# Performance work log

Hardware: AMD Instinct MI355X
Metric: run time of the kernel (lower is better)

Reference implementation:

```python
import jax, jax.numpy as jnp
import numpy as np

BN_EPS = 1e-5


def setup_inputs() -> dict:
    key = jax.random.key(0)
    ks = jax.random.split(key, 10)
    N, E, D = 100000, 1600000, 64
    node_feats = jax.random.normal(ks[0], (N, D), dtype=jnp.float32)
    edge_feats = jax.random.randint(ks[1], (E, 3), 0, 2, dtype=jnp.int64)
    edge_index = jax.random.randint(ks[2], (2, E), 0, N, dtype=jnp.int64)
    return {
        "node_feats": node_feats,
        "edge_feats": edge_feats,
        "edge_index": edge_index,
        "num_nodes": N,
        "num_edges": E,
        "eps": jnp.zeros((1,), jnp.float32),
        "bond_emb0": jax.random.normal(ks[3], (5, D), dtype=jnp.float32) * 0.05,
        "bond_emb1": jax.random.normal(ks[4], (6, D), dtype=jnp.float32) * 0.05,
        "bond_emb2": jax.random.normal(ks[5], (2, D), dtype=jnp.float32) * 0.05,
        "W1": jax.random.normal(ks[6], (2 * D, D), dtype=jnp.float32) * (1.0 / np.sqrt(D)),
        "b1": jnp.zeros((2 * D,), jnp.float32),
        "gamma": jnp.ones((2 * D,), jnp.float32),
        "beta": jnp.zeros((2 * D,), jnp.float32),
        "W2": jax.random.normal(ks[7], (D, 2 * D), dtype=jnp.float32) * (1.0 / np.sqrt(2 * D)),
        "b2": jnp.zeros((D,), jnp.float32),
    }


def reference(node_feats, edge_feats, edge_index, num_nodes, num_edges,
              eps, bond_emb0, bond_emb1, bond_emb2,
              W1, b1, gamma, beta, W2, b2):
    # BondEncoder: sum of categorical embeddings over 3 bond features -> [E, D]
    edge_emb = (bond_emb0[edge_feats[:, 0]]
                + bond_emb1[edge_feats[:, 1]]
                + bond_emb2[edge_feats[:, 2]])
    # gather source-node feats (edge_index[1]), combine, relu -> [E, D]
    message = jax.nn.relu(node_feats[edge_index[1]] + edge_emb)
    # scatter_add into target nodes (edge_index[0]) -> [N, D]
    message_reduce = jax.ops.segment_sum(message, edge_index[0], num_segments=num_nodes)
    h = (1.0 + eps) * node_feats + message_reduce  # eps shape [1] broadcasts
    # MLP: Linear -> BatchNorm1d (training-mode batch stats) -> ReLU -> Linear
    h1 = h @ W1.T + b1  # [N, 2D]
    mean = jnp.mean(h1, axis=0)
    var = jnp.mean(jnp.square(h1 - mean), axis=0)  # biased variance (torch BN)
    h1 = gamma * (h1 - mean) * jax.lax.rsqrt(var + BN_EPS) + beta
    h1 = jax.nn.relu(h1)
    return h1 @ W2.T + b2  # [N, D]
```

## Files before the change

kernel.cpp:

```cpp
#include <hip/hip_runtime.h>
#include <stdint.h>

#define D    64
#define D2   128
#define R    98
#define NBK  1024
#define CAP  2176

__global__ void k_embsum(
    const float* __restrict__ be0, const float* __restrict__ be1,
    const float* __restrict__ be2, float* __restrict__ embsum,
    int* __restrict__ bcursor, float* __restrict__ Mbar)
{
    int c = blockIdx.x;
    int t = threadIdx.x;
    if (c < 60) {
        int f0 = c / 12;
        int r  = c % 12;
        int f1 = r / 2;
        int f2 = r % 2;
        embsum[c * D + t] = be0[f0 * D + t] + be1[f1 * D + t] + be2[f2 * D + t];
    } else if (c < 76) {
        int i = (c - 60) * 64 + t;
        if (i < NBK) bcursor[i * 16] = i * CAP;
    } else {
        int i = (c - 76) * 64 + t;
        Mbar[i] = 0.0f;
    }
}

__global__ __launch_bounds__(512) void k_part(
    const int* __restrict__ ei, const int* __restrict__ ef,
    int* __restrict__ bcursor, int* __restrict__ payload, int E)
{
    __shared__ int scnt[NBK];
    __shared__ int sstart[NBK];
    __shared__ int sgbase[NBK];
    __shared__ int sdat[4096];
    __shared__ unsigned short sbkt[4096];
    __shared__ int sred2[512];

    int t = threadIdx.x;
    for (int i = t; i < NBK; i += 512) scnt[i] = 0;
    __syncthreads();

    int base2 = blockIdx.x * 2048;

    int b0[4], p0[4], r0[4];
    int b1[4], p1[4], r1[4];

    #pragma unroll
    for (int k = 0; k < 4; k++) {
        int i2 = base2 + k * 512 + t;
        int e0 = i2 * 2;
        if (e0 < E) {
            int2 d  = ((const int2*)ei)[i2];
            int2 s  = ((const int2*)(ei + E))[i2];
            int2 q0 = ((const int2*)ef)[3 * i2 + 0];
            int2 q1 = ((const int2*)ef)[3 * i2 + 1];
            int2 q2 = ((const int2*)ef)[3 * i2 + 2];
            {
                int bb = d.x / R; if (bb > NBK - 1) bb = NBK - 1;
                int ld = d.x - bb * R;
                int code = q0.x * 12 + q0.y * 2 + q1.x;
                b0[k] = bb;
                p0[k] = s.x | (code << 17) | (ld << 23);
                r0[k] = atomicAdd(&scnt[bb], 1);
            }
            if (e0 + 1 < E) {
                int bb = d.y / R; if (bb > NBK - 1) bb = NBK - 1;
                int ld = d.y - bb * R;
                int code = q1.y * 12 + q2.x * 2 + q2.y;
                b1[k] = bb;
                p1[k] = s.y | (code << 17) | (ld << 23);
                r1[k] = atomicAdd(&scnt[bb], 1);
            }
        }
    }
    __syncthreads();

    int c0 = scnt[t * 2], c1 = scnt[t * 2 + 1];
    sred2[t] = c0 + c1;
    __syncthreads();
    int sv = sred2[t];
    for (int off = 1; off < 512; off <<= 1) {
        int x = (t >= off) ? sred2[t - off] : 0;
        __syncthreads();
        sred2[t] += x;
        __syncthreads();
    }
    int excl = sred2[t] - sv;
    sstart[t * 2]     = excl;
    sstart[t * 2 + 1] = excl + c0;
    __syncthreads();

    for (int i = t; i < NBK; i += 512) {
        int c = scnt[i];
        if (c) sgbase[i] = atomicAdd(&bcursor[i * 16], c);
    }
    __syncthreads();

    #pragma unroll
    for (int k = 0; k < 4; k++) {
        int i2 = base2 + k * 512 + t;
        int e0 = i2 * 2;
        if (e0 < E) {
            int slot = sstart[b0[k]] + r0[k];
            sdat[slot] = p0[k]; sbkt[slot] = (unsigned short)b0[k];
            if (e0 + 1 < E) {
                slot = sstart[b1[k]] + r1[k];
                sdat[slot] = p1[k]; sbkt[slot] = (unsigned short)b1[k];
            }
        }
    }
    __syncthreads();

    int tc = E - base2 * 2; if (tc > 4096) tc = 4096;
    #pragma unroll
    for (int k = 0; k < 8; k++) {
        int i = k * 512 + t;
        if (i < tc) {
            int bb = sbkt[i];
            int pos = sgbase[bb] + (i - sstart[bb]);
            if (pos < (bb + 1) * CAP) payload[pos] = sdat[i];
        }
    }
}

__global__ __launch_bounds__(512, 8) void k_sortred(
    const float* __restrict__ nf,
    const int* __restrict__ bcursor,
    int* __restrict__ payload,
    const float* __restrict__ embsum,
    const float* __restrict__ epsp,
    float* __restrict__ h, int N)
{
    __shared__ float sE[60 * D];
    __shared__ int   sq[CAP];
    __shared__ int   scn[R + 1];
    __shared__ int   scur[R];
    __shared__ int   sscan[128];

    int tid = threadIdx.x;
    int b = blockIdx.x;
    int n0 = b * R;

    for (int i = tid; i < 60 * D; i += 512) sE[i] = embsum[i];
    if (tid <= R) scn[tid] = 0;
    __syncthreads();

    int js = b * CAP;
    int cnt = bcursor[b * 16] - js;
    if (cnt > CAP) cnt = CAP;
    if (cnt < 0) cnt = 0;

    for (int i = tid; i < cnt; i += 512)
        atomicAdd(&scn[((unsigned)payload[js + i] >> 23) + 1], 1);
    __syncthreads();

    if (tid < 128) sscan[tid] = (tid <= R) ? scn[tid] : 0;
    __syncthreads();
    for (int off = 1; off < 128; off <<= 1) {
        int x = 0;
        if (tid < 128 && tid >= off) x = sscan[tid - off];
        __syncthreads();
        if (tid < 128) sscan[tid] += x;
        __syncthreads();
    }
    if (tid <= R) {
        scn[tid] = sscan[tid];
        if (tid < R) scur[tid] = sscan[tid];
    }
    __syncthreads();

    for (int i = tid; i < cnt; i += 512) {
        int u = payload[js + i];
        int pos = atomicAdd(&scur[(unsigned)u >> 23], 1);
        sq[pos] = u;
    }
    __syncthreads();

    int w = tid >> 6, l = tid & 63;
    float epsv = 1.0f + epsp[0];
    for (int r = w; r < R; r += 8) {
        int n = n0 + r;
        if (n >= N) break;
        int st = scn[r], en = scn[r + 1];
        float acc = 0.0f;
        for (int jb = st; jb < en; jb += 64) {
            int u = (jb + l < en) ? sq[jb + l] : 0;
            int m = en - jb; if (m > 64) m = 64;
            int t = 0;
            for (; t + 8 <= m; t += 8) {
                int a0 = __shfl(u, t + 0);
                int a1 = __shfl(u, t + 1);
                int a2 = __shfl(u, t + 2);
                int a3 = __shfl(u, t + 3);
                int a4 = __shfl(u, t + 4);
                int a5 = __shfl(u, t + 5);
                int a6 = __shfl(u, t + 6);
                int a7 = __shfl(u, t + 7);
                float x0 = nf[(size_t)(a0 & 0x1FFFF) * D + l];
                float x1 = nf[(size_t)(a1 & 0x1FFFF) * D + l];
                float x2 = nf[(size_t)(a2 & 0x1FFFF) * D + l];
                float x3 = nf[(size_t)(a3 & 0x1FFFF) * D + l];
                float x4 = nf[(size_t)(a4 & 0x1FFFF) * D + l];
                float x5 = nf[(size_t)(a5 & 0x1FFFF) * D + l];
                float x6 = nf[(size_t)(a6 & 0x1FFFF) * D + l];
                float x7 = nf[(size_t)(a7 & 0x1FFFF) * D + l];
                float e0 = sE[((a0 >> 17) & 63) * D + l];
                float e1 = sE[((a1 >> 17) & 63) * D + l];
                float e2 = sE[((a2 >> 17) & 63) * D + l];
                float e3 = sE[((a3 >> 17) & 63) * D + l];
                float e4 = sE[((a4 >> 17) & 63) * D + l];
                float e5 = sE[((a5 >> 17) & 63) * D + l];
                float e6 = sE[((a6 >> 17) & 63) * D + l];
                float e7 = sE[((a7 >> 17) & 63) * D + l];
                acc += fmaxf(x0 + e0, 0.0f) + fmaxf(x1 + e1, 0.0f)
                     + fmaxf(x2 + e2, 0.0f) + fmaxf(x3 + e3, 0.0f)
                     + fmaxf(x4 + e4, 0.0f) + fmaxf(x5 + e5, 0.0f)
                     + fmaxf(x6 + e6, 0.0f) + fmaxf(x7 + e7, 0.0f);
            }
            for (; t + 4 <= m; t += 4) {
                int a0 = __shfl(u, t + 0);
                int a1 = __shfl(u, t + 1);
                int a2 = __shfl(u, t + 2);
                int a3 = __shfl(u, t + 3);
                float x0 = nf[(size_t)(a0 & 0x1FFFF) * D + l];
                float x1 = nf[(size_t)(a1 & 0x1FFFF) * D + l];
                float x2 = nf[(size_t)(a2 & 0x1FFFF) * D + l];
                float x3 = nf[(size_t)(a3 & 0x1FFFF) * D + l];
                float e0 = sE[((a0 >> 17) & 63) * D + l];
                float e1 = sE[((a1 >> 17) & 63) * D + l];
                float e2 = sE[((a2 >> 17) & 63) * D + l];
                float e3 = sE[((a3 >> 17) & 63) * D + l];
                acc += fmaxf(x0 + e0, 0.0f) + fmaxf(x1 + e1, 0.0f)
                     + fmaxf(x2 + e2, 0.0f) + fmaxf(x3 + e3, 0.0f);
            }
            for (; t < m; t++) {
                int a = __shfl(u, t);
                acc += fmaxf(nf[(size_t)(a & 0x1FFFF) * D + l]
                             + sE[((a >> 17) & 63) * D + l], 0.0f);
            }
        }
        h[(size_t)n * D + l] = fmaf(epsv, nf[(size_t)n * D + l], acc);
    }
    __syncthreads();

    float* P = (float*)(payload + (size_t)b * CAP);
    const float4* h4 = (const float4*)h;
    if (tid < 256) {
        int iB = tid >> 4, jB = tid & 15;
        float M[4][4];
        #pragma unroll
        for (int a = 0; a < 4; a++)
            #pragma unroll
            for (int c = 0; c < 4; c++) M[a][c] = 0.0f;
        #pragma unroll 2
        for (int n2 = 0; n2 < R; n2++) {
            int n = n0 + n2;
            if (n >= N) break;
            float4 a = h4[(size_t)n * 16 + iB];
            float4 c = h4[(size_t)n * 16 + jB];
            M[0][0] = fmaf(a.x, c.x, M[0][0]);
            M[0][1] = fmaf(a.x, c.y, M[0][1]);
            M[0][2] = fmaf(a.x, c.z, M[0][2]);
            M[0][3] = fmaf(a.x, c.w, M[0][3]);
            M[1][0] = fmaf(a.y, c.x, M[1][0]);
            M[1][1] = fmaf(a.y, c.y, M[1][1]);
            M[1][2] = fmaf(a.y, c.z, M[1][2]);
            M[1][3] = fmaf(a.y, c.w, M[1][3]);
            M[2][0] = fmaf(a.z, c.x, M[2][0]);
            M[2][1] = fmaf(a.z, c.y, M[2][1]);
            M[2][2] = fmaf(a.z, c.z, M[2][2]);
            M[2][3] = fmaf(a.z, c.w, M[2][3]);
            M[3][0] = fmaf(a.w, c.x, M[3][0]);
            M[3][1] = fmaf(a.w, c.y, M[3][1]);
            M[3][2] = fmaf(a.w, c.z, M[3][2]);
            M[3][3] = fmaf(a.w, c.w, M[3][3]);
        }
        #pragma unroll
        for (int a = 0; a < 4; a++)
            #pragma unroll
            for (int c = 0; c < 4; c++) {
                int gi = iB * 4 + a, gj = jB * 4 + c;
                if (gi <= gj)
                    P[gi * 64 + gj - ((gi * (gi + 1)) >> 1)] = M[a][c];
            }
    } else if (tid < 320) {
        int lc = tid - 256;
        float s = 0.0f;
        for (int n2 = 0; n2 < R; n2++) {
            int n = n0 + n2;
            if (n >= N) break;
            s += h[(size_t)n * D + lc];
        }
        P[2080 + lc] = s;
    }
}

__global__ __launch_bounds__(512) void k_redM(
    const float* __restrict__ pM,
    float* __restrict__ Mbar, float invN)
{
    __shared__ float sred[512];
    int tid = threadIdx.x;
    int eq = tid & 63, bq = tid >> 6;
    int ec = blockIdx.x >> 2;
    int qg = blockIdx.x & 3;
    int e  = ec * 64 + eq;

    int src;
    if (e < 4096) {
        int i = e >> 6, j = e & 63;
        int a = i < j ? i : j;
        int b2 = i < j ? j : i;
        src = a * 64 + b2 - ((a * (a + 1)) >> 1);
    } else {
        src = 2080 + (e - 4096);
    }

    int bbase = qg * 256;
    float s0 = 0.0f, s1 = 0.0f, s2 = 0.0f, s3 = 0.0f;
    for (int b = bq; b < 256; b += 32) {
        s0 += pM[(size_t)(bbase + b +  0) * CAP + src];
        s1 += pM[(size_t)(bbase + b +  8) * CAP + src];
        s2 += pM[(size_t)(bbase + b + 16) * CAP + src];
        s3 += pM[(size_t)(bbase + b + 24) * CAP + src];
    }
    sred[tid] = (s0 + s1) + (s2 + s3);
    __syncthreads();
    if (tid < 64) {
        float s = 0.0f;
        #pragma unroll
        for (int q = 0; q < 8; q++) s += sred[q * 64 + tid];
        atomicAdd(&Mbar[e], s * invN);
    }
}

__global__ __launch_bounds__(64) void k_bn(
    const float* __restrict__ Mbar,
    const float* __restrict__ W1,
    const float* __restrict__ b1,
    const float* __restrict__ gamma, const float* __restrict__ beta,
    float* __restrict__ ss)
{
    int c = blockIdx.x;
    int k = threadIdx.x;

    float wk = W1[c * D + k];
    float dk = wk * Mbar[4096 + k];

    float tk = 0.0f;
    #pragma unroll 8
    for (int j = 0; j < 64; j++)
        tk = fmaf(Mbar[k * 64 + j], W1[c * D + j], tk);
    float qk = wk * tk;

    #pragma unroll
    for (int off = 32; off > 0; off >>= 1) {
        dk += __shfl_xor(dk, off);
        qk += __shfl_xor(qk, off);
    }

    if (k == 0) {
        float var  = fmaxf(qk - dk * dk, 0.0f);
        float mean = dk + b1[c];
        float sc   = gamma[c] * rsqrtf(var + 1e-5f);
        ss[c]       = sc;
        ss[128 + c] = beta[c] - mean * sc;
    }
}

#define ABS 132
__global__ __launch_bounds__(512) void k_gemm2(
    const float* __restrict__ h,
    const float* __restrict__ W1,
    const float* __restrict__ b1,
    const float* __restrict__ ss,
    const float* __restrict__ W2,
    const float* __restrict__ b2v,
    float* __restrict__ out,
    int N, int tiles)
{
    __shared__ float AB[128 * ABS];
    __shared__ float W1t[64 * 128];
    __shared__ float W2t[128 * 64];

    int tid = threadIdx.x;

    {
        int c  = tid >> 2;
        int k0 = (tid & 3) * 16;
        const float4* wr = (const float4*)(W1 + c * D + k0);
        #pragma unroll
        for (int q = 0; q < 4; q++) {
            float4 u = wr[q];
            int k = k0 + q * 4;
            W1t[(k + 0) * 128 + c] = u.x;
            W1t[(k + 1) * 128 + c] = u.y;
            W1t[(k + 2) * 128 + c] = u.z;
            W1t[(k + 3) * 128 + c] = u.w;
        }
    }
    {
        int j  = tid >> 3;
        int k0 = (tid & 7) * 16;
        const float4* wr = (const float4*)(W2 + j * D2 + k0);
        #pragma unroll
        for (int q = 0; q < 4; q++) {
            float4 u = wr[q];
            int k = k0 + q * 4;
            W2t[(k + 0) * 64 + j] = u.x;
            W2t[(k + 1) * 64 + j] = u.y;
            W2t[(k + 2) * 64 + j] = u.z;
            W2t[(k + 3) * 64 + j] = u.w;
        }
    }

    int rg = tid >> 5, cg = tid & 31;
    float bb0 = b1[cg * 4 + 0];
    float bb1 = b1[cg * 4 + 1];
    float bb2 = b1[cg * 4 + 2];
    float bb3 = b1[cg * 4 + 3];
    float4 scv = *(const float4*)&ss[cg * 4];
    float4 shv = *(const float4*)&ss[128 + cg * 4];

    int r2 = tid >> 4, c2 = tid & 15;
    float4 obv = *(const float4*)&b2v[c2 * 4];

    int sr = tid >> 2;
    int sc16 = (tid & 3) * 16;

    float4 pf[4];
    #pragma unroll
    for (int q = 0; q < 4; q++) pf[q] = make_float4(0.f, 0.f, 0.f, 0.f);
    {
        int gr = blockIdx.x * 128 + sr;
        if (gr < N) {
            const float4* hrow = (const float4*)(h + (size_t)gr * D + sc16);
            #pragma unroll
            for (int q = 0; q < 4; q++) pf[q] = hrow[q];
        }
    }

    for (int t = blockIdx.x; t < tiles; t += gridDim.x) {
        int row0 = t * 128;
        __syncthreads();
        {
            float* dstp = &AB[sr * ABS + sc16];
            #pragma unroll
            for (int q = 0; q < 4; q++) ((float4*)dstp)[q] = pf[q];
        }
        __syncthreads();

        float acc[8][4];
        #pragma unroll
        for (int i = 0; i < 8; i++)
            #pragma unroll
            for (int j = 0; j < 4; j++) acc[i][j] = 0.0f;

        #pragma unroll 2
        for (int k4 = 0; k4 < 16; k4++) {
            float4 w0 = *(const float4*)&W1t[(k4 * 4 + 0) * 128 + cg * 4];
            float4 w1 = *(const float4*)&W1t[(k4 * 4 + 1) * 128 + cg * 4];
            float4 w2 = *(const float4*)&W1t[(k4 * 4 + 2) * 128 + cg * 4];
            float4 w3 = *(const float4*)&W1t[(k4 * 4 + 3) * 128 + cg * 4];
            #pragma unroll
            for (int i = 0; i < 8; i++) {
                float4 a = *(const float4*)&AB[(rg * 8 + i) * ABS + k4 * 4];
                acc[i][0] = fmaf(a.x, w0.x, acc[i][0]);
                acc[i][1] = fmaf(a.x, w0.y, acc[i][1]);
                acc[i][2] = fmaf(a.x, w0.z, acc[i][2]);
                acc[i][3] = fmaf(a.x, w0.w, acc[i][3]);
                acc[i][0] = fmaf(a.y, w1.x, acc[i][0]);
                acc[i][1] = fmaf(a.y, w1.y, acc[i][1]);
                acc[i][2] = fmaf(a.y, w1.z, acc[i][2]);
                acc[i][3] = fmaf(a.y, w1.w, acc[i][3]);
                acc[i][0] = fmaf(a.z, w2.x, acc[i][0]);
                acc[i][1] = fmaf(a.z, w2.y, acc[i][1]);
                acc[i][2] = fmaf(a.z, w2.z, acc[i][2]);
                acc[i][3] = fmaf(a.z, w2.w, acc[i][3]);
                acc[i][0] = fmaf(a.w, w3.x, acc[i][0]);
                acc[i][1] = fmaf(a.w, w3.y, acc[i][1]);
                acc[i][2] = fmaf(a.w, w3.z, acc[i][2]);
                acc[i][3] = fmaf(a.w, w3.w, acc[i][3]);
            }
        }
        __syncthreads();

        int tn = t + gridDim.x;
        #pragma unroll
        for (int q = 0; q < 4; q++) pf[q] = make_float4(0.f, 0.f, 0.f, 0.f);
        if (tn < tiles) {
            int gr = tn * 128 + sr;
            if (gr < N) {
                const float4* hrow = (const float4*)(h + (size_t)gr * D + sc16);
                #pragma unroll
                for (int q = 0; q < 4; q++) pf[q] = hrow[q];
            }
        }

        #pragma unroll
        for (int i = 0; i < 8; i++) {
            float g0 = fmaxf(fmaf(acc[i][0] + bb0, scv.x, shv.x), 0.0f);
            float g1 = fmaxf(fmaf(acc[i][1] + bb1, scv.y, shv.y), 0.0f);
            float g2 = fmaxf(fmaf(acc[i][2] + bb2, scv.z, shv.z), 0.0f);
            float g3 = fmaxf(fmaf(acc[i][3] + bb3, scv.w, shv.w), 0.0f);
            *(float4*)&AB[(rg * 8 + i) * ABS + cg * 4] = make_float4(g0, g1, g2, g3);
        }
        __syncthreads();

        float acc2[4][4];
        #pragma unroll
        for (int i = 0; i < 4; i++)
            #pragma unroll
            for (int j = 0; j < 4; j++) acc2[i][j] = 0.0f;

        #pragma unroll 2
        for (int k4 = 0; k4 < 32; k4++) {
            float4 u0 = *(const float4*)&W2t[(k4 * 4 + 0) * 64 + c2 * 4];
            float4 u1 = *(const float4*)&W2t[(k4 * 4 + 1) * 64 + c2 * 4];
            float4 u2 = *(const float4*)&W2t[(k4 * 4 + 2) * 64 + c2 * 4];
            float4 u3 = *(const float4*)&W2t[(k4 * 4 + 3) * 64 + c2 * 4];
            #pragma unroll
            for (int i = 0; i < 4; i++) {
                float4 g = *(const float4*)&AB[(r2 * 4 + i) * ABS + k4 * 4];
                acc2[i][0] = fmaf(g.x, u0.x, acc2[i][0]);
                acc2[i][1] = fmaf(g.x, u0.y, acc2[i][1]);
                acc2[i][2] = fmaf(g.x, u0.z, acc2[i][2]);
                acc2[i][3] = fmaf(g.x, u0.w, acc2[i][3]);
                acc2[i][0] = fmaf(g.y, u1.x, acc2[i][0]);
                acc2[i][1] = fmaf(g.y, u1.y, acc2[i][1]);
                acc2[i][2] = fmaf(g.y, u1.z, acc2[i][2]);
                acc2[i][3] = fmaf(g.y, u1.w, acc2[i][3]);
                acc2[i][0] = fmaf(g.z, u2.x, acc2[i][0]);
                acc2[i][1] = fmaf(g.z, u2.y, acc2[i][1]);
                acc2[i][2] = fmaf(g.z, u2.z, acc2[i][2]);
                acc2[i][3] = fmaf(g.z, u2.w, acc2[i][3]);
                acc2[i][0] = fmaf(g.w, u3.x, acc2[i][0]);
                acc2[i][1] = fmaf(g.w, u3.y, acc2[i][1]);
                acc2[i][2] = fmaf(g.w, u3.z, acc2[i][2]);
                acc2[i][3] = fmaf(g.w, u3.w, acc2[i][3]);
            }
        }

        #pragma unroll
        for (int i = 0; i < 4; i++) {
            int gr = row0 + r2 * 4 + i;
            if (gr < N) {
                float4 pk = make_float4(acc2[i][0] + obv.x, acc2[i][1] + obv.y,
                                        acc2[i][2] + obv.z, acc2[i][3] + obv.w);
                *(float4*)&out[(size_t)gr * D + c2 * 4] = pk;
            }
        }
    }
}

extern "C" void kernel_launch(void* const* d_in, const int* in_sizes, int n_in,
                              void* d_out, int out_size, void* d_ws, size_t ws_size,
                              hipStream_t stream)
{
    const float* nf    = (const float*)d_in[0];
    const int*   ef    = (const int*)d_in[1];
    const int*   ei    = (const int*)d_in[2];
    const float* epsp  = (const float*)d_in[5];
    const float* be0   = (const float*)d_in[6];
    const float* be1   = (const float*)d_in[7];
    const float* be2   = (const float*)d_in[8];
    const float* W1    = (const float*)d_in[9];
    const float* b1    = (const float*)d_in[10];
    const float* gamma = (const float*)d_in[11];
    const float* beta  = (const float*)d_in[12];
    const float* W2    = (const float*)d_in[13];
    const float* b2v   = (const float*)d_in[14];
    float*       out   = (float*)d_out;

    int N = in_sizes[0] / D;
    int E = in_sizes[1] / 3;

    int tiles2 = (N + 127) / 128;

    float* h       = (float*)d_ws;
    float* Mbar    = h + (size_t)N * D;
    float* ss      = Mbar + 4224;
    float* embsum  = ss + 256;
    int*   bcursor = (int*)(embsum + 60 * D);
    int*   payload = bcursor + NBK * 16;
    float* pM      = (float*)payload;

    k_embsum<<<142, 64, 0, stream>>>(be0, be1, be2, embsum, bcursor, Mbar);

    int E2 = (E + 1) / 2;
    int gP = (E2 + 2047) / 2048;
    k_part<<<gP, 512, 0, stream>>>(ei, ef, bcursor, payload, E);

    k_sortred<<<NBK, 512, 0, stream>>>(nf, bcursor, payload, embsum, epsp, h, N);

    k_redM<<<260, 512, 0, stream>>>(pM, Mbar, 1.0f / (float)N);
    k_bn<<<128, 64, 0, stream>>>(Mbar, W1, b1, gamma, beta, ss);

    k_gemm2<<<256, 512, 0, stream>>>(h, W1, b1, ss, W2, b2v, out, N, tiles2);
}
```

Before: 306.5 us.

## Pre-transpose MLP weights globally, restructure GEMM tiling to wave-uniform weight loads

The W1/W2 transposes move into the setup kernel, which writes them to global workspace, so the fused MLP kernel no longer stages weights in LDS. Each wave now owns a fixed column slice and reads its weights as wave-uniform global loads that hit cache. Each thread handles two rows, and the grid doubles because LDS use per block drops. The edge partition kernel also switches to 8 contiguous edges per thread with int4 vector loads. The risk is higher per-thread register pressure and extra global traffic for the weight reads.

```diff
diff --git a/kernel.cpp b/kernel.cpp
--- a/kernel.cpp
+++ b/kernel.cpp
@@ -10,7 +10,9 @@
 __global__ void k_embsum(
     const float* __restrict__ be0, const float* __restrict__ be1,
     const float* __restrict__ be2, float* __restrict__ embsum,
-    int* __restrict__ bcursor, float* __restrict__ Mbar)
+    int* __restrict__ bcursor, float* __restrict__ Mbar,
+    const float* __restrict__ W1, const float* __restrict__ W2,
+    float* __restrict__ W1tg, float* __restrict__ W2tg)
 {
     int c = blockIdx.x;
     int t = threadIdx.x;
@@ -23,9 +25,16 @@
     } else if (c < 76) {
         int i = (c - 60) * 64 + t;
         if (i < NBK) bcursor[i * 16] = i * CAP;
-    } else {
+    } else if (c < 142) {
         int i = (c - 76) * 64 + t;
         Mbar[i] = 0.0f;
+    } else if (c < 270) {
+        int ch = c - 142;
+        W1tg[t * 128 + ch] = W1[ch * D + t];
+    } else {
+        int j = c - 270;
+        W2tg[t * 64 + j]        = W2[j * D2 + t];
+        W2tg[(t + 64) * 64 + j] = W2[j * D2 + t + 64];
     }
 }
 
@@ -44,37 +53,52 @@
     for (int i = t; i < NBK; i += 512) scnt[i] = 0;
     __syncthreads();
 
-    int base2 = blockIdx.x * 2048;
-
-    int b0[4], p0[4], r0[4];
-    int b1[4], p1[4], r1[4];
+    int e0 = blockIdx.x * 4096 + t * 8;
+    int dd[8], sv[8], fa[8], fb[8], fc[8];
+    int bk[8], pk[8], rk[8];
+
+    if (e0 + 8 <= E) {
+        int4 dA = *(const int4*)(ei + e0);
+        int4 dB = *(const int4*)(ei + e0 + 4);
+        int4 sA = *(const int4*)(ei + (size_t)E + e0);
+        int4 sB = *(const int4*)(ei + (size_t)E + e0 + 4);
+        const int4* fp = (const int4*)(ef + (size_t)e0 * 3);
+        int4 g0 = fp[0], g1 = fp[1], g2 = fp[2];
+        int4 g3 = fp[3], g4 = fp[4], g5 = fp[5];
+        dd[0]=dA.x; dd[1]=dA.y; dd[2]=dA.z; dd[3]=dA.w;
+        dd[4]=dB.x; dd[5]=dB.y; dd[6]=dB.z; dd[7]=dB.w;
+        sv[0]=sA.x; sv[1]=sA.y; sv[2]=sA.z; sv[3]=sA.w;
+        sv[4]=sB.x; sv[5]=sB.y; sv[6]=sB.z; sv[7]=sB.w;
+        fa[0]=g0.x; fb[0]=g0.y; fc[0]=g0.z;
+        fa[1]=g0.w; fb[1]=g1.x; fc[1]=g1.y;
+        fa[2]=g1.z; fb[2]=g1.w; fc[2]=g2.x;
+        fa[3]=g2.y; fb[3]=g2.z; fc[3]=g2.w;
+        fa[4]=g3.x; fb[4]=g3.y; fc[4]=g3.z;
+        fa[5]=g3.w; fb[5]=g4.x; fc[5]=g4.y;
+        fa[6]=g4.z; fb[6]=g4.w; fc[6]=g5.x;
+        fa[7]=g5.y; fb[7]=g5.z; fc[7]=g5.w;
+    } else {
+        #pragma unroll
+        for (int k = 0; k < 8; k++) {
+            if (e0 + k < E) {
+                dd[k] = ei[e0 + k];
+                sv[k] = ei[(size_t)E + e0 + k];
+                fa[k] = ef[(size_t)(e0 + k) * 3 + 0];
+                fb[k] = ef[(size_t)(e0 + k) * 3 + 1];
+                fc[k] = ef[(size_t)(e0 + k) * 3 + 2];
+            }
+        }
+    }
 
     #pragma unroll
-    for (int k = 0; k < 4; k++) {
-        int i2 = base2 + k * 512 + t;
-        int e0 = i2 * 2;
-        if (e0 < E) {
-            int2 d  = ((const int2*)ei)[i2];
-            int2 s  = ((const int2*)(ei + E))[i2];
-            int2 q0 = ((const int2*)ef)[3 * i2 + 0];
-            int2 q1 = ((const int2*)ef)[3 * i2 + 1];
-            int2 q2 = ((const int2*)ef)[3 * i2 + 2];
-            {
-                int bb = d.x / R; if (bb > NBK - 1) bb = NBK - 1;
-                int ld = d.x - bb * R;
-                int code = q0.x * 12 + q0.y * 2 + q1.x;
-                b0[k] = bb;
-                p0[k] = s.x | (code << 17) | (ld << 23);
-                r0[k] = atomicAdd(&scnt[bb], 1);
-            }
-            if (e0 + 1 < E) {
-                int bb = d.y / R; if (bb > NBK - 1) bb = NBK - 1;
-                int ld = d.y - bb * R;
-                int code = q1.y * 12 + q2.x * 2 + q2.y;
-                b1[k] = bb;
-                p1[k] = s.y | (code << 17) | (ld << 23);
-                r1[k] = atomicAdd(&scnt[bb], 1);
-            }
+    for (int k = 0; k < 8; k++) {
+        if (e0 + k < E) {
+            int bb = dd[k] / R; if (bb > NBK - 1) bb = NBK - 1;
+            int ld = dd[k] - bb * R;
+            int code = fa[k] * 12 + fb[k] * 2 + fc[k];
+            bk[k] = bb;
+            pk[k] = sv[k] | (code << 17) | (ld << 23);
+            rk[k] = atomicAdd(&scnt[bb], 1);
         }
     }
     __syncthreads();
@@ -82,14 +106,14 @@
     int c0 = scnt[t * 2], c1 = scnt[t * 2 + 1];
     sred2[t] = c0 + c1;
     __syncthreads();
-    int sv = sred2[t];
+    int svv = sred2[t];
     for (int off = 1; off < 512; off <<= 1) {
         int x = (t >= off) ? sred2[t - off] : 0;
         __syncthreads();
         sred2[t] += x;
         __syncthreads();
     }
-    int excl = sred2[t] - sv;
+    int excl = sred2[t] - svv;
     sstart[t * 2]     = excl;
     sstart[t * 2 + 1] = excl + c0;
     __syncthreads();
@@ -101,21 +125,15 @@
     __syncthreads();
 
     #pragma unroll
-    for (int k = 0; k < 4; k++) {
-        int i2 = base2 + k * 512 + t;
-        int e0 = i2 * 2;
-        if (e0 < E) {
-            int slot = sstart[b0[k]] + r0[k];
-            sdat[slot] = p0[k]; sbkt[slot] = (unsigned short)b0[k];
-            if (e0 + 1 < E) {
-                slot = sstart[b1[k]] + r1[k];
-                sdat[slot] = p1[k]; sbkt[slot] = (unsigned short)b1[k];
-            }
-        }
-    }
-    __syncthreads();
-
-    int tc = E - base2 * 2; if (tc > 4096) tc = 4096;
+    for (int k = 0; k < 8; k++) {
+        if (e0 + k < E) {
+            int slot = sstart[bk[k]] + rk[k];
+            sdat[slot] = pk[k]; sbkt[slot] = (unsigned short)bk[k];
+        }
+    }
+    __syncthreads();
+
+    int tc = E - blockIdx.x * 4096; if (tc > 4096) tc = 4096;
     #pragma unroll
     for (int k = 0; k < 8; k++) {
         int i = k * 512 + t;
@@ -375,61 +393,23 @@
 #define ABS 132
 __global__ __launch_bounds__(512) void k_gemm2(
     const float* __restrict__ h,
-    const float* __restrict__ W1,
+    const float* __restrict__ W1tg,
     const float* __restrict__ b1,
     const float* __restrict__ ss,
-    const float* __restrict__ W2,
+    const float* __restrict__ W2tg,
     const float* __restrict__ b2v,
     float* __restrict__ out,
     int N, int tiles)
 {
     __shared__ float AB[128 * ABS];
-    __shared__ float W1t[64 * 128];
-    __shared__ float W2t[128 * 64];
 
     int tid = threadIdx.x;
-
-    {
-        int c  = tid >> 2;
-        int k0 = (tid & 3) * 16;
-        const float4* wr = (const float4*)(W1 + c * D + k0);
-        #pragma unroll
-        for (int q = 0; q < 4; q++) {
-            float4 u = wr[q];
-            int k = k0 + q * 4;
-            W1t[(k + 0) * 128 + c] = u.x;
-            W1t[(k + 1) * 128 + c] = u.y;
-            W1t[(k + 2) * 128 + c] = u.z;
-            W1t[(k + 3) * 128 + c] = u.w;
-        }
-    }
-    {
-        int j  = tid >> 3;
-        int k0 = (tid & 7) * 16;
-        const float4* wr = (const float4*)(W2 + j * D2 + k0);
-        #pragma unroll
-        for (int q = 0; q < 4; q++) {
-            float4 u = wr[q];
-            int k = k0 + q * 4;
-            W2t[(k + 0) * 64 + j] = u.x;
-            W2t[(k + 1) * 64 + j] = u.y;
-            W2t[(k + 2) * 64 + j] = u.z;
-            W2t[(k + 3) * 64 + j] = u.w;
-        }
-    }
-
-    int rg = tid >> 5, cg = tid & 31;
-    float bb0 = b1[cg * 4 + 0];
-    float bb1 = b1[cg * 4 + 1];
-    float bb2 = b1[cg * 4 + 2];
-    float bb3 = b1[cg * 4 + 3];
-    float4 scv = *(const float4*)&ss[cg * 4];
-    float4 shv = *(const float4*)&ss[128 + cg * 4];
-
-    int r2 = tid >> 4, c2 = tid & 15;
-    float4 obv = *(const float4*)&b2v[c2 * 4];
-
-    int sr = tid >> 2;
+    int l   = tid & 63;
+    int wv  = tid >> 6;
+    int cg0 = wv * 16;
+    int oc0 = wv * 8;
+
+    int sr   = tid >> 2;
     int sc16 = (tid & 3) * 16;
 
     float4 pf[4];
@@ -454,37 +434,53 @@
         }
         __syncthreads();
 
-        float acc[8][4];
-        #pragma unroll
-        for (int i = 0; i < 8; i++)
-            #pragma unroll
-            for (int j = 0; j < 4; j++) acc[i][j] = 0.0f;
+        float acc0[16], acc1[16];
+        #pragma unroll
+        for (int c = 0; c < 16; c++) { acc0[c] = 0.0f; acc1[c] = 0.0f; }
 
         #pragma unroll 2
         for (int k4 = 0; k4 < 16; k4++) {
-            float4 w0 = *(const float4*)&W1t[(k4 * 4 + 0) * 128 + cg * 4];
-            float4 w1 = *(const float4*)&W1t[(k4 * 4 + 1) * 128 + cg * 4];
-            float4 w2 = *(const float4*)&W1t[(k4 * 4 + 2) * 128 + cg * 4];
-            float4 w3 = *(const float4*)&W1t[(k4 * 4 + 3) * 128 + cg * 4];
+            float4 a0 = *(const float4*)&AB[l * ABS + k4 * 4];
+            float4 a1 = *(const float4*)&AB[(l + 64) * ABS + k4 * 4];
+            float a0v[4] = {a0.x, a0.y, a0.z, a0.w};
+            float a1v[4] = {a1.x, a1.y, a1.z, a1.w};
             #pragma unroll
-            for (int i = 0; i < 8; i++) {
-                float4 a = *(const float4*)&AB[(rg * 8 + i) * ABS + k4 * 4];
-                acc[i][0] = fmaf(a.x, w0.x, acc[i][0]);
-                acc[i][1] = fmaf(a.x, w0.y, acc[i][1]);
-                acc[i][2] = fmaf(a.x, w0.z, acc[i][2]);
-                acc[i][3] = fmaf(a.x, w0.w, acc[i][3]);
-                acc[i][0] = fmaf(a.y, w1.x, acc[i][0]);
-                acc[i][1] = fmaf(a.y, w1.y, acc[i][1]);
-                acc[i][2] = fmaf(a.y, w1.z, acc[i][2]);
-                acc[i][3] = fmaf(a.y, w1.w, acc[i][3]);
-                acc[i][0] = fmaf(a.z, w2.x, acc[i][0]);
-                acc[i][1] = fmaf(a.z, w2.y, acc[i][1]);
-                acc[i][2] = fmaf(a.z, w2.z, acc[i][2]);
-                acc[i][3] = fmaf(a.z, w2.w, acc[i][3]);
-                acc[i][0] = fmaf(a.w, w3.x, acc[i][0]);
-                acc[i][1] = fmaf(a.w, w3.y, acc[i][1]);
-                acc[i][2] = fmaf(a.w, w3.z, acc[i][2]);
-                acc[i][3] = fmaf(a.w, w3.w, acc[i][3]);
+            for (int kk = 0; kk < 4; kk++) {
+                const float4* wr = (const float4*)(W1tg + (size_t)(k4 * 4 + kk) * 128 + cg0);
+                float4 wA = wr[0], wB = wr[1], wC = wr[2], wD = wr[3];
+                float fa0 = a0v[kk], fa1 = a1v[kk];
+                acc0[ 0] = fmaf(fa0, wA.x, acc0[ 0]);
+                acc0[ 1] = fmaf(fa0, wA.y, acc0[ 1]);
+                acc0[ 2] = fmaf(fa0, wA.z, acc0[ 2]);
+                acc0[ 3] = fmaf(fa0, wA.w, acc0[ 3]);
+                acc0[ 4] = fmaf(fa0, wB.x, acc0[ 4]);
+                acc0[ 5] = fmaf(fa0, wB.y, acc0[ 5]);
+                acc0[ 6] = fmaf(fa0, wB.z, acc0[ 6]);
+                acc0[ 7] = fmaf(fa0, wB.w, acc0[ 7]);
+                acc0[ 8] = fmaf(fa0, wC.x, acc0[ 8]);
+                acc0[ 9] = fmaf(fa0, wC.y, acc0[ 9]);
+                acc0[10] = fmaf(fa0, wC.z, acc0[10]);
+                acc0[11] = fmaf(fa0, wC.w, acc0[11]);
+                acc0[12] = fmaf(fa0, wD.x, acc0[12]);
+                acc0[13] = fmaf(fa0, wD.y, acc0[13]);
+                acc0[14] = fmaf(fa0, wD.z, acc0[14]);
+                acc0[15] = fmaf(fa0, wD.w, acc0[15]);
+                acc1[ 0] = fmaf(fa1, wA.x, acc1[ 0]);
+                acc1[ 1] = fmaf(fa1, wA.y, acc1[ 1]);
+                acc1[ 2] = fmaf(fa1, wA.z, acc1[ 2]);
+                acc1[ 3] = fmaf(fa1, wA.w, acc1[ 3]);
+                acc1[ 4] = fmaf(fa1, wB.x, acc1[ 4]);
+                acc1[ 5] = fmaf(fa1, wB.y, acc1[ 5]);
+                acc1[ 6] = fmaf(fa1, wB.z, acc1[ 6]);
+                acc1[ 7] = fmaf(fa1, wB.w, acc1[ 7]);
+                acc1[ 8] = fmaf(fa1, wC.x, acc1[ 8]);
+                acc1[ 9] = fmaf(fa1, wC.y, acc1[ 9]);
+                acc1[10] = fmaf(fa1, wC.z, acc1[10]);
+                acc1[11] = fmaf(fa1, wC.w, acc1[11]);
+                acc1[12] = fmaf(fa1, wD.x, acc1[12]);
+                acc1[13] = fmaf(fa1, wD.y, acc1[13]);
+                acc1[14] = fmaf(fa1, wD.z, acc1[14]);
+                acc1[15] = fmaf(fa1, wD.w, acc1[15]);
             }
         }
         __syncthreads();
@@ -502,57 +498,72 @@
         }
 
         #pragma unroll
-        for (int i = 0; i < 8; i++) {
-            float g0 = fmaxf(fmaf(acc[i][0] + bb0, scv.x, shv.x), 0.0f);
-            float g1 = fmaxf(fmaf(acc[i][1] + bb1, scv.y, shv.y), 0.0f);
-            float g2 = fmaxf(fmaf(acc[i][2] + bb2, scv.z, shv.z), 0.0f);
-            float g3 = fmaxf(fmaf(acc[i][3] + bb3, scv.w, shv.w), 0.0f);
-            *(float4*)&AB[(rg * 8 + i) * ABS + cg * 4] = make_float4(g0, g1, g2, g3);
-        }
-        __syncthreads();
-
-        float acc2[4][4];
-        #pragma unroll
-        for (int i = 0; i < 4; i++)
-            #pragma unroll
-            for (int j = 0; j < 4; j++) acc2[i][j] = 0.0f;
+        for (int q = 0; q < 4; q++) {
+            float4 bb4 = *(const float4*)&b1[cg0 + q * 4];
+            float4 sc4 = *(const float4*)&ss[cg0 + q * 4];
+            float4 sh4 = *(const float4*)&ss[128 + cg0 + q * 4];
+            float4 gA, gB;
+            gA.x = fmaxf(fmaf(acc0[q*4+0] + bb4.x, sc4.x, sh4.x), 0.0f);
+            gA.y = fmaxf(fmaf(acc0[q*4+1] + bb4.y, sc4.y, sh4.y), 0.0f);
+            gA.z = fmaxf(fmaf(acc0[q*4+2] + bb4.z, sc4.z, sh4.z), 0.0f);
+            gA.w = fmaxf(fmaf(acc0[q*4+3] + bb4.w, sc4.w, sh4.w), 0.0f);
+            gB.x = fmaxf(fmaf(acc1[q*4+0] + bb4.x, sc4.x, sh4.x), 0.0f);
+            gB.y = fmaxf(fmaf(acc1[q*4+1] + bb4.y, sc4.y, sh4.y), 0.0f);
+            gB.z = fmaxf(fmaf(acc1[q*4+2] + bb4.z, sc4.z, sh4.z), 0.0f);
+            gB.w = fmaxf(fmaf(acc1[q*4+3] + bb4.w, sc4.w, sh4.w), 0.0f);
+            *(float4*)&AB[l * ABS + cg0 + q * 4]        = gA;
+            *(float4*)&AB[(l + 64) * ABS + cg0 + q * 4] = gB;
+        }
+        __syncthreads();
+
+        float c20[8], c21[8];
+        #pragma unroll
+        for (int c = 0; c < 8; c++) { c20[c] = 0.0f; c21[c] = 0.0f; }
 
         #pragma unroll 2
         for (int k4 = 0; k4 < 32; k4++) {
-            float4 u0 = *(const float4*)&W2t[(k4 * 4 + 0) * 64 + c2 * 4];
-            float4 u1 = *(const float4*)&W2t[(k4 * 4 + 1) * 64 + c2 * 4];
-            float4 u2 = *(const float4*)&W2t[(k4 * 4 + 2) * 64 + c2 * 4];
-            float4 u3 = *(const float4*)&W2t[(k4 * 4 + 3) * 64 + c2 * 4];
+            float4 g0 = *(const float4*)&AB[l * ABS + k4 * 4];
+            float4 g1 = *(const float4*)&AB[(l + 64) * ABS + k4 * 4];
+            float g0v[4] = {g0.x, g0.y, g0.z, g0.w};
+            float g1v[4] = {g1.x, g1.y, g1.z, g1.w};
             #pragma unroll
-            for (int i = 0; i < 4; i++) {
-                float4 g = *(const float4*)&AB[(r2 * 4 + i) * ABS + k4 * 4];
-                acc2[i][0] = fmaf(g.x, u0.x, acc2[i][0]);
-                acc2[i][1] = fmaf(g.x, u0.y, acc2[i][1]);
-                acc2[i][2] = fmaf(g.x, u0.z, acc2[i][2]);
-                acc2[i][3] = fmaf(g.x, u0.w, acc2[i][3]);
-                acc2[i][0] = fmaf(g.y, u1.x, acc2[i][0]);
-                acc2[i][1] = fmaf(g.y, u1.y, acc2[i][1]);
-                acc2[i][2] = fmaf(g.y, u1.z, acc2[i][2]);
-                acc2[i][3] = fmaf(g.y, u1.w, acc2[i][3]);
-                acc2[i][0] = fmaf(g.z, u2.x, acc2[i][0]);
-                acc2[i][1] = fmaf(g.z, u2.y, acc2[i][1]);
-                acc2[i][2] = fmaf(g.z, u2.z, acc2[i][2]);
-                acc2[i][3] = fmaf(g.z, u2.w, acc2[i][3]);
-                acc2[i][0] = fmaf(g.w, u3.x, acc2[i][0]);
-                acc2[i][1] = fmaf(g.w, u3.y, acc2[i][1]);
-                acc2[i][2] = fmaf(g.w, u3.z, acc2[i][2]);
-                acc2[i][3] = fmaf(g.w, u3.w, acc2[i][3]);
-            }
-        }
-
-        #pragma unroll
-        for (int i = 0; i < 4; i++) {
-            int gr = row0 + r2 * 4 + i;
-            if (gr < N) {
-                float4 pk = make_float4(acc2[i][0] + obv.x, acc2[i][1] + obv.y,
-                                        acc2[i][2] + obv.z, acc2[i][3] + obv.w);
-                *(float4*)&out[(size_t)gr * D + c2 * 4] = pk;
-            }
+            for (int kk = 0; kk < 4; kk++) {
+                const float4* ur = (const float4*)(W2tg + (size_t)(k4 * 4 + kk) * 64 + oc0);
+                float4 uA = ur[0], uB = ur[1];
+                float f0_ = g0v[kk], f1_ = g1v[kk];
+                c20[0] = fmaf(f0_, uA.x, c20[0]);
+                c20[1] = fmaf(f0_, uA.y, c20[1]);
+                c20[2] = fmaf(f0_, uA.z, c20[2]);
+                c20[3] = fmaf(f0_, uA.w, c20[3]);
+                c20[4] = fmaf(f0_, uB.x, c20[4]);
+                c20[5] = fmaf(f0_, uB.y, c20[5]);
+                c20[6] = fmaf(f0_, uB.z, c20[6]);
+                c20[7] = fmaf(f0_, uB.w, c20[7]);
+                c21[0] = fmaf(f1_, uA.x, c21[0]);
+                c21[1] = fmaf(f1_, uA.y, c21[1]);
+                c21[2] = fmaf(f1_, uA.z, c21[2]);
+                c21[3] = fmaf(f1_, uA.w, c21[3]);
+                c21[4] = fmaf(f1_, uB.x, c21[4]);
+                c21[5] = fmaf(f1_, uB.y, c21[5]);
+                c21[6] = fmaf(f1_, uB.z, c21[6]);
+                c21[7] = fmaf(f1_, uB.w, c21[7]);
+            }
+        }
+
+        float4 obA = *(const float4*)&b2v[oc0];
+        float4 obB = *(const float4*)&b2v[oc0 + 4];
+        int gr0 = row0 + l, gr1 = row0 + l + 64;
+        if (gr0 < N) {
+            *(float4*)&out[(size_t)gr0 * D + oc0] =
+                make_float4(c20[0] + obA.x, c20[1] + obA.y, c20[2] + obA.z, c20[3] + obA.w);
+            *(float4*)&out[(size_t)gr0 * D + oc0 + 4] =
+                make_float4(c20[4] + obB.x, c20[5] + obB.y, c20[6] + obB.z, c20[7] + obB.w);
+        }
+        if (gr1 < N) {
+            *(float4*)&out[(size_t)gr1 * D + oc0] =
+                make_float4(c21[0] + obA.x, c21[1] + obA.y, c21[2] + obA.z, c21[3] + obA.w);
+            *(float4*)&out[(size_t)gr1 * D + oc0 + 4] =
+                make_float4(c21[4] + obB.x, c21[5] + obB.y, c21[6] + obB.z, c21[7] + obB.w);
         }
     }
 }
@@ -585,14 +596,16 @@
     float* Mbar    = h + (size_t)N * D;
     float* ss      = Mbar + 4224;
     float* embsum  = ss + 256;
-    int*   bcursor = (int*)(embsum + 60 * D);
+    float* W1tg    = embsum + 60 * D;
+    float* W2tg    = W1tg + 8192;
+    int*   bcursor = (int*)(W2tg + 8192);
     int*   payload = bcursor + NBK * 16;
     float* pM      = (float*)payload;
 
-    k_embsum<<<142, 64, 0, stream>>>(be0, be1, be2, embsum, bcursor, Mbar);
-
-    int E2 = (E + 1) / 2;
-    int gP = (E2 + 2047) / 2048;
+    k_embsum<<<334, 64, 0, stream>>>(be0, be1, be2, embsum, bcursor, Mbar,
+                                     W1, W2, W1tg, W2tg);
+
+    int gP = (E + 4095) / 4096;
     k_part<<<gP, 512, 0, stream>>>(ei, ef, bcursor, payload, E);
 
     k_sortred<<<NBK, 512, 0, stream>>>(nf, bcursor, payload, embsum, epsp, h, N);
@@ -600,5 +613,5 @@
     k_redM<<<260, 512, 0, stream>>>(pM, Mbar, 1.0f / (float)N);
     k_bn<<<128, 64, 0, stream>>>(Mbar, W1, b1, gamma, beta, ss);
 
-    k_gemm2<<<256, 512, 0, stream>>>(h, W1, b1, ss, W2, b2v, out, N, tiles2);
+    k_gemm2<<<512, 512, 0, stream>>>(h, W1tg, b1, ss, W2tg, b2v, out, N, tiles2);
 }
```

Result: slower. 377.2 us (+23.1%).
